# Kernel optimization log

Measured on AMD Instinct MI355X. Metric: run time of the kernel, lower is better.

## Reference

```python
import jax, jax.numpy as jnp
import numpy as np

DIM, E_DIM, HID = 512, 1024, 256
N_EXP, N_MIC, TOP_K, TOP_K_MIC = 8, 325, 2, 8
EPS_LN = 1e-5


def _layernorm(x, g, b):
    mu = x.mean(-1, keepdims=True)
    var = ((x - mu) ** 2).mean(-1, keepdims=True)
    return (x - mu) / jnp.sqrt(var + EPS_LN) * g + b


def setup_inputs() -> dict:
    key = jax.random.key(0)
    ks = jax.random.split(key, 20)
    s = 0.02
    return {
        "x": jax.random.normal(ks[0], (2, 512, DIM), jnp.float32),
        "router_w": jax.random.normal(ks[1], (N_EXP, DIM), jnp.float32) * s,
        "router_b": jnp.zeros((N_EXP,), jnp.float32),
        "exp_w1": jax.random.normal(ks[2], (N_EXP, E_DIM, DIM), jnp.float32) * s,
        "exp_b1": jnp.zeros((N_EXP, E_DIM), jnp.float32),
        "exp_w2": jax.random.normal(ks[3], (N_EXP, DIM, E_DIM), jnp.float32) * s,
        "exp_b2": jnp.zeros((N_EXP, DIM), jnp.float32),
        "mrouter_w": jax.random.normal(ks[4], (N_MIC, DIM), jnp.float32) * s,
        "mrouter_b": jnp.zeros((N_MIC,), jnp.float32),
        "mic_w1": jax.random.normal(ks[5], (N_MIC, HID, DIM), jnp.float32) * s,
        "mic_b1": jnp.zeros((N_MIC, HID), jnp.float32),
        "mic_w2": jax.random.normal(ks[6], (N_MIC, DIM, HID), jnp.float32) * s,
        "mic_b2": jnp.zeros((N_MIC, DIM), jnp.float32),
        "mic_g": jnp.ones((N_MIC, DIM), jnp.float32),
        "mic_beta": jnp.zeros((N_MIC, DIM), jnp.float32),
        "norm_g": jnp.ones((DIM,), jnp.float32),
        "norm_b": jnp.zeros((DIM,), jnp.float32),
    }


def _forward(x, router_w, router_b, exp_w1, exp_b1, exp_w2, exp_b2,
             mrouter_w, mrouter_b, mic_w1, mic_b1, mic_w2, mic_b2,
             mic_g, mic_beta, norm_g, norm_b):
    B, S, D = x.shape
    xf = x.reshape(-1, D)  # [T, D]

    # ---- expert routing (top-2 of 8) ----
    probs = jax.nn.softmax(xf @ router_w.T + router_b, axis=-1)
    topp, topi = jax.lax.top_k(probs, TOP_K)
    topp = topp / (topp.sum(-1, keepdims=True) + 1e-8)

    # dense compute over 8 experts, combine with top-k weights
    h = jax.nn.gelu(jnp.einsum('td,ehd->teh', xf, exp_w1) + exp_b1, approximate=False)
    ye = jnp.einsum('teh,edh->ted', h, exp_w2) + exp_b2  # [T, E, D]
    comb_w = (jax.nn.one_hot(topi, N_EXP, dtype=xf.dtype) * topp[..., None]).sum(1)  # [T, E]
    eo = jnp.einsum('te,ted->td', comb_w, ye)

    # ---- micro routing (top-8 of 325) ----
    mprobs = jax.nn.softmax(eo @ mrouter_w.T + mrouter_b, axis=-1)
    mtopp, mtopi = jax.lax.top_k(mprobs, TOP_K_MIC)
    mtopp = mtopp / (mtopp.sum(-1, keepdims=True) + 1e-8)

    def micro_slot(eo, p, idx):
        # gather per-token micro params, batched GEMV dispatch
        hm = jax.nn.gelu(jnp.einsum('td,thd->th', eo, mic_w1[idx]) + mic_b1[idx],
                         approximate=False)
        ym = jnp.einsum('th,tdh->td', hm, mic_w2[idx]) + mic_b2[idx]
        n = _layernorm(eo + ym, mic_g[idx], mic_beta[idx])
        return p[:, None] * n

    micro_slot = jax.checkpoint(micro_slot, static_argnums=())
    mo = jnp.zeros_like(eo)
    for k in range(TOP_K_MIC):  # small fixed loop over slots
        mo = mo + micro_slot(eo, mtopp[:, k], mtopi[:, k])

    combined = (eo + 0.1 * mo).reshape(B, S, D)
    return _layernorm(combined, norm_g, norm_b)


def reference(x, router_w, router_b, exp_w1, exp_b1, exp_w2, exp_b2,
              mrouter_w, mrouter_b, mic_w1, mic_b1, mic_w2, mic_b2,
              mic_g, mic_beta, norm_g, norm_b):
    return _forward(x, router_w, router_b, exp_w1, exp_b1, exp_w2, exp_b2,
                    mrouter_w, mrouter_b, mic_w1, mic_b1, mic_w2, mic_b2,
                    mic_g, mic_beta, norm_g, norm_b)
```

## Files before the change

kernel.cpp:

```cpp
#include <hip/hip_runtime.h>
#include <hip/hip_bf16.h>
#include <math.h>

#define T_TOK 1024
#define DIMM  512
#define EDIM  1024
#define HIDD  256
#define NEXP  8
#define NMIC  325
#define E8TILES 264
#define MTILES  840

typedef __attribute__((ext_vector_type(8))) short bf16x8;
typedef __attribute__((ext_vector_type(4))) float f32x4;

__device__ __forceinline__ float dot4(float4 a, float4 b) {
    return a.x*b.x + a.y*b.y + a.z*b.z + a.w*b.w;
}
__device__ __forceinline__ float gelu_exact(float x) {
    return 0.5f * x * (1.0f + erff(x * 0.70710678118654752f));
}
__device__ __forceinline__ float wave_sum(float v) {
    #pragma unroll
    for (int o = 32; o; o >>= 1) v += __shfl_xor(v, o);
    return v;
}
__device__ __forceinline__ short f2bf(float f) {
    union { __hip_bfloat16 h; short s; } u;
    u.h = __float2bfloat16(f);
    return u.s;
}
__device__ __forceinline__ bf16x8 cvt8(float4 a, float4 b) {
    bf16x8 r;
    r[0]=f2bf(a.x); r[1]=f2bf(a.y); r[2]=f2bf(a.z); r[3]=f2bf(a.w);
    r[4]=f2bf(b.x); r[5]=f2bf(b.y); r[6]=f2bf(b.z); r[7]=f2bf(b.w);
    return r;
}

__global__ void k_router(const float* __restrict__ x, const float* __restrict__ rw,
                         const float* __restrict__ rb, int* __restrict__ eidx,
                         float* __restrict__ ew, int* __restrict__ ecnt) {
    int wave = threadIdx.x >> 6, lane = threadIdx.x & 63;
    int t = blockIdx.x * 4 + wave;
    if (t >= T_TOK) return;
    const float* xr = x + (size_t)t * DIMM;
    float xv[8];
    #pragma unroll
    for (int j = 0; j < 8; ++j) xv[j] = xr[lane + 64*j];
    float p[NEXP];
    #pragma unroll
    for (int e = 0; e < NEXP; ++e) {
        const float* wr = rw + (size_t)e * DIMM;
        float a = 0.f;
        #pragma unroll
        for (int j = 0; j < 8; ++j) a += xv[j] * wr[lane + 64*j];
        p[e] = wave_sum(a) + rb[e];
    }
    float m = p[0];
    #pragma unroll
    for (int e = 1; e < NEXP; ++e) m = fmaxf(m, p[e]);
    float Z = 0.f;
    #pragma unroll
    for (int e = 0; e < NEXP; ++e) { p[e] = expf(p[e] - m); Z += p[e]; }
    #pragma unroll
    for (int e = 0; e < NEXP; ++e) p[e] /= Z;
    int i1 = 0; float v1 = p[0];
    #pragma unroll
    for (int e = 1; e < NEXP; ++e) if (p[e] > v1) { v1 = p[e]; i1 = e; }
    int i2 = -1; float v2 = -1.f;
    #pragma unroll
    for (int e = 0; e < NEXP; ++e) if (e != i1 && p[e] > v2) { v2 = p[e]; i2 = e; }
    float s = v1 + v2 + 1e-8f;
    if (lane == 0) {
        eidx[t*2] = i1; eidx[t*2+1] = i2;
        ew[t*2] = v1 / s; ew[t*2+1] = v2 / s;
        atomicAdd(&ecnt[i1], 1); atomicAdd(&ecnt[i2], 1);
    }
}

__global__ void k_scan(const int* __restrict__ cnt, int n, int pm,
                       int* __restrict__ off, int* __restrict__ cur,
                       int2* __restrict__ tiles, int* __restrict__ ntile) {
    __shared__ int s[512], s2[512];
    int tid = threadIdx.x;
    int v  = (tid < n) ? cnt[tid] : 0;
    int tc = (v + pm - 1) / pm;
    s[tid] = v; s2[tid] = tc;
    __syncthreads();
    for (int d = 1; d < 512; d <<= 1) {
        int a = (tid >= d) ? s[tid-d] : 0;
        int b = (tid >= d) ? s2[tid-d] : 0;
        __syncthreads();
        s[tid] += a; s2[tid] += b;
        __syncthreads();
    }
    int myoff = s[tid] - v, tb = s2[tid] - tc;
    if (tid < n) { off[tid] = myoff; cur[tid] = myoff; }
    if (tid == n-1) off[n] = s[tid];
    if (tid == 511) *ntile = s2[511];
    for (int j = 0; j < tc; ++j) tiles[tb + j] = make_int2(tid, myoff + j*pm);
}

__global__ void k_scatter(const int* __restrict__ idx, const float* __restrict__ w,
                          int total, int S, int* __restrict__ cur,
                          int* __restrict__ ptok, float* __restrict__ pw) {
    int g = blockIdx.x * blockDim.x + threadIdx.x;
    if (g >= total) return;
    int t = g / S;
    int e = idx[g];
    int pos = atomicAdd(&cur[e], 1);
    ptok[pos] = t; pw[pos] = w[g];
}

__global__ __launch_bounds__(256) void k_effn1(
    const float* __restrict__ x, const float* __restrict__ w1, const float* __restrict__ b1,
    const int2* __restrict__ tiles, const int* __restrict__ ntile,
    const int* __restrict__ eoff, const int* __restrict__ ep_tok,
    float* __restrict__ hbuf) {
    if ((int)blockIdx.x >= *ntile) return;
    int2 tl = tiles[blockIdx.x];
    int e = tl.x, pbase = tl.y;
    int m = min(8, eoff[e+1] - pbase);
    __shared__ float4 xs[8][128];
    __shared__ int tok_s[8];
    int tid = threadIdx.x;
    if (tid < 8) tok_s[tid] = ep_tok[pbase + ((tid < m) ? tid : 0)];
    __syncthreads();
    const float4* x4 = (const float4*)x;
    for (int q = tid; q < 8*128; q += 256) {
        int i = q >> 7, k = q & 127;
        xs[i][k] = x4[(size_t)tok_s[i] * 128 + k];
    }
    __syncthreads();
    int c = blockIdx.y * 256 + tid;
    const float4* wr = (const float4*)(w1 + ((size_t)e * EDIM + c) * DIMM);
    float acc[8];
    #pragma unroll
    for (int i = 0; i < 8; ++i) acc[i] = 0.f;
    for (int kk = 0; kk < 128; ++kk) {
        float4 wv = wr[kk];
        #pragma unroll
        for (int i = 0; i < 8; ++i) acc[i] += dot4(wv, xs[i][kk]);
    }
    float bb = b1[(size_t)e * EDIM + c];
    for (int i = 0; i < m; ++i)
        hbuf[(size_t)(pbase + i) * EDIM + c] = gelu_exact(acc[i] + bb);
}

__global__ __launch_bounds__(256) void k_effn2(
    const float* __restrict__ hbuf, const float* __restrict__ w2, const float* __restrict__ b2,
    const int2* __restrict__ tiles, const int* __restrict__ ntile,
    const int* __restrict__ eoff, const int* __restrict__ ep_tok, const float* __restrict__ ep_w,
    float* __restrict__ eo) {
    if ((int)blockIdx.x >= *ntile) return;
    int2 tl = tiles[blockIdx.x];
    int e = tl.x, pbase = tl.y;
    int m = min(8, eoff[e+1] - pbase);
    int kc = blockIdx.z;
    __shared__ float4 hs[8][128];
    __shared__ int tok_s[8];
    __shared__ float pw_s[8];
    int tid = threadIdx.x;
    if (tid < 8) {
        int ok = tid < m;
        tok_s[tid] = ok ? ep_tok[pbase + tid] : 0;
        pw_s[tid]  = ok ? ep_w[pbase + tid] : 0.f;
    }
    __syncthreads();
    const float4* h4 = (const float4*)hbuf;
    for (int q = tid; q < 8*128; q += 256) {
        int i = q >> 7, k = q & 127;
        hs[i][k] = h4[(size_t)(pbase + ((i < m) ? i : 0)) * 256 + kc * 128 + k];
    }
    __syncthreads();
    int c = blockIdx.y * 256 + tid;
    const float4* wr = (const float4*)(w2 + ((size_t)e * DIMM + c) * EDIM + (size_t)kc * 512);
    float acc[8];
    #pragma unroll
    for (int i = 0; i < 8; ++i) acc[i] = 0.f;
    for (int kk = 0; kk < 128; ++kk) {
        float4 wv = wr[kk];
        #pragma unroll
        for (int i = 0; i < 8; ++i) acc[i] += dot4(wv, hs[i][kk]);
    }
    float bb = (kc == 0) ? b2[(size_t)e * DIMM + c] : 0.f;
    for (int i = 0; i < m; ++i) {
        float val = (acc[i] + bb) * pw_s[i];
        atomicAdd(&eo[(size_t)tok_s[i] * DIMM + c], val);
    }
}

__global__ __launch_bounds__(384) void k_mlog(
    const float* __restrict__ eo, const float* __restrict__ mw, const float* __restrict__ mb,
    float* __restrict__ mlog) {
    int t0 = blockIdx.x * 4;
    __shared__ float4 es[4][128];
    int tid = threadIdx.x;
    const float4* eo4 = (const float4*)eo;
    for (int q = tid; q < 4*128; q += 384) {
        int i = q >> 7, k = q & 127;
        es[i][k] = eo4[(size_t)(t0 + i) * 128 + k];
    }
    __syncthreads();
    if (tid < NMIC) {
        const float4* wr = (const float4*)(mw + (size_t)tid * DIMM);
        float acc[4] = {0.f, 0.f, 0.f, 0.f};
        for (int kk = 0; kk < 128; ++kk) {
            float4 wv = wr[kk];
            #pragma unroll
            for (int i = 0; i < 4; ++i) acc[i] += dot4(wv, es[i][kk]);
        }
        float bb = mb[tid];
        #pragma unroll
        for (int i = 0; i < 4; ++i) mlog[(size_t)(t0 + i) * NMIC + tid] = acc[i] + bb;
    }
}

__global__ void k_mtop(const float* __restrict__ mlog, int* __restrict__ mtopi,
                       float* __restrict__ mtopp, int* __restrict__ mcnt) {
    int wave = threadIdx.x >> 6, lane = threadIdx.x & 63;
    int t = blockIdx.x * 4 + wave;
    if (t >= T_TOK) return;
    float v[6]; int vi[6];
    #pragma unroll
    for (int j = 0; j < 6; ++j) {
        int n = lane + 64*j;
        vi[j] = n;
        v[j] = (n < NMIC) ? mlog[(size_t)t * NMIC + n] : -1e30f;
    }
    float M = v[0];
    #pragma unroll
    for (int j = 1; j < 6; ++j) M = fmaxf(M, v[j]);
    #pragma unroll
    for (int o = 32; o; o >>= 1) M = fmaxf(M, __shfl_xor(M, o));
    float Z = 0.f;
    #pragma unroll
    for (int j = 0; j < 6; ++j) Z += expf(v[j] - M);
    Z = wave_sum(Z);
    float bk[8]; int bi[8];
    for (int k = 0; k < 8; ++k) {
        float lv = v[0]; int li = vi[0];
        #pragma unroll
        for (int j = 1; j < 6; ++j)
            if (v[j] > lv) { lv = v[j]; li = vi[j]; }
        #pragma unroll
        for (int o = 32; o; o >>= 1) {
            float ov = __shfl_xor(lv, o); int oi = __shfl_xor(li, o);
            if (ov > lv || (ov == lv && oi < li)) { lv = ov; li = oi; }
        }
        bk[k] = expf(lv - M) / Z; bi[k] = li;
        #pragma unroll
        for (int j = 0; j < 6; ++j) if (vi[j] == li) v[j] = -1e30f;
    }
    float s = 0.f;
    #pragma unroll
    for (int k = 0; k < 8; ++k) s += bk[k];
    s += 1e-8f;
    if (lane == 0) {
        for (int k = 0; k < 8; ++k) {
            mtopi[t*8 + k] = bi[k];
            mtopp[t*8 + k] = bk[k] / s;
            atomicAdd(&mcnt[bi[k]], 1);
        }
    }
}

__global__ __launch_bounds__(256, 4) void k_micro(
    const float* __restrict__ eo, const float* __restrict__ w1, const float* __restrict__ b1,
    const float* __restrict__ w2, const float* __restrict__ b2,
    const float* __restrict__ g, const float* __restrict__ beta,
    const int2* __restrict__ tiles, const int* __restrict__ ntile,
    const int* __restrict__ moff, const int* __restrict__ mp_tok, const float* __restrict__ mp_w,
    float* __restrict__ mo) {
    if ((int)blockIdx.x >= *ntile) return;
    int2 tl = tiles[blockIdx.x];
    int mi = tl.x, pbase = tl.y;
    int pm = min(16, moff[mi+1] - pbase);
    __shared__ __align__(16) char smem[34816];
    short* hf  = (short*)smem;
    short* eof = (short*)(smem + 8192);
    float* R   = (float*)smem;
    __shared__ int tok_s[16];
    __shared__ float pw_s[16];
    int tid = threadIdx.x;
    if (tid < 16) {
        int ok = tid < pm;
        tok_s[tid] = mp_tok[pbase + (ok ? tid : 0)];
        pw_s[tid]  = ok ? mp_w[pbase + tid] : 0.f;
    }
    __syncthreads();
    int m0 = tid & 15;
    const float4* eorow = (const float4*)(eo + (size_t)tok_s[m0] * DIMM);
    for (int kk = tid >> 4; kk < 128; kk += 16) {
        float4 v = eorow[kk];
        int off = ((kk >> 3) * 512) + ((((kk >> 1) & 3) * 16 + m0) * 8) + ((kk & 1) * 4);
        short4 s4; s4.x = f2bf(v.x); s4.y = f2bf(v.y); s4.z = f2bf(v.z); s4.w = f2bf(v.w);
        *(short4*)(eof + off) = s4;
    }
    __syncthreads();
    int wave = tid >> 6, lane = tid & 63;
    int quad = lane >> 4, lcol = lane & 15;
    f32x4 zero = {0.f, 0.f, 0.f, 0.f};
    f32x4 accA[4];
    #pragma unroll
    for (int q = 0; q < 4; ++q) accA[q] = zero;
    const float* w1base = w1 + (size_t)mi * HIDD * DIMM;
    for (int ks = 0; ks < 16; ++ks) {
        bf16x8 a = *(bf16x8*)(eof + ks*512 + lane*8);
        int kb = ks*32 + quad*8;
        #pragma unroll
        for (int q = 0; q < 4; ++q) {
            int n = wave*64 + q*16 + lcol;
            const float* wp = w1base + (size_t)n * DIMM + kb;
            float4 wa = *(const float4*)wp;
            float4 wb = *(const float4*)(wp + 4);
            accA[q] = __builtin_amdgcn_mfma_f32_16x16x32_bf16(a, cvt8(wa, wb), accA[q], 0, 0, 0);
        }
    }
    #pragma unroll
    for (int q = 0; q < 4; ++q) {
        int h = wave*64 + q*16 + lcol;
        float bb = b1[(size_t)mi * HIDD + h];
        int obase = ((h >> 5) * 512) + (((h >> 3) & 3) * 16) * 8 + (h & 7);
        #pragma unroll
        for (int r = 0; r < 4; ++r) {
            int mm = quad*4 + r;
            hf[obase + mm*8] = f2bf(gelu_exact(accA[q][r] + bb));
        }
    }
    __syncthreads();
    f32x4 accB[8];
    #pragma unroll
    for (int q = 0; q < 8; ++q) accB[q] = zero;
    const float* w2base = w2 + (size_t)mi * DIMM * HIDD;
    for (int ks = 0; ks < 8; ++ks) {
        bf16x8 a = *(bf16x8*)(hf + ks*512 + lane*8);
        int kb = ks*32 + quad*8;
        #pragma unroll
        for (int q = 0; q < 8; ++q) {
            int d = wave*128 + q*16 + lcol;
            const float* wp = w2base + (size_t)d * HIDD + kb;
            float4 wa = *(const float4*)wp;
            float4 wb = *(const float4*)(wp + 4);
            accB[q] = __builtin_amdgcn_mfma_f32_16x16x32_bf16(a, cvt8(wa, wb), accB[q], 0, 0, 0);
        }
    }
    __syncthreads();
    #pragma unroll
    for (int q = 0; q < 8; ++q) {
        int d = wave*128 + q*16 + lcol;
        float bb = b2[(size_t)mi * DIMM + d];
        #pragma unroll
        for (int r = 0; r < 4; ++r) {
            int mm = quad*4 + r;
            R[mm*520 + d] = accB[q][r] + bb;
        }
    }
    __syncthreads();
    for (int i = wave; i < pm; i += 4) {
        int t = tok_s[i];
        const float* eort = eo + (size_t)t * DIMM;
        float vv[8];
        float sum = 0.f;
        #pragma unroll
        for (int j = 0; j < 8; ++j) {
            int d = lane + 64*j;
            vv[j] = R[i*520 + d] + eort[d];
            sum += vv[j];
        }
        sum = wave_sum(sum);
        float mu = sum * (1.f/512.f);
        float var = 0.f;
        #pragma unroll
        for (int j = 0; j < 8; ++j) { float d0 = vv[j] - mu; var += d0*d0; }
        var = wave_sum(var) * (1.f/512.f);
        float rstd = rsqrtf(var + 1e-5f);
        float p = pw_s[i];
        #pragma unroll
        for (int j = 0; j < 8; ++j) {
            int d = lane + 64*j;
            float nj = (vv[j] - mu) * rstd * g[(size_t)mi * DIMM + d] + beta[(size_t)mi * DIMM + d];
            atomicAdd(&mo[(size_t)t * DIMM + d], p * nj);
        }
    }
}

__global__ void k_final(const float* __restrict__ eo, const float* __restrict__ mo,
                        const float* __restrict__ g, const float* __restrict__ b,
                        float* __restrict__ out) {
    int wave = threadIdx.x >> 6, lane = threadIdx.x & 63;
    int t = blockIdx.x * 4 + wave;
    if (t >= T_TOK) return;
    float vv[8];
    float sum = 0.f;
    #pragma unroll
    for (int j = 0; j < 8; ++j) {
        int d = lane + 64*j;
        vv[j] = eo[(size_t)t * DIMM + d] + 0.1f * mo[(size_t)t * DIMM + d];
        sum += vv[j];
    }
    sum = wave_sum(sum);
    float mu = sum * (1.f/512.f);
    float var = 0.f;
    #pragma unroll
    for (int j = 0; j < 8; ++j) { float d0 = vv[j] - mu; var += d0*d0; }
    var = wave_sum(var) * (1.f/512.f);
    float rstd = rsqrtf(var + 1e-5f);
    #pragma unroll
    for (int j = 0; j < 8; ++j) {
        int d = lane + 64*j;
        out[(size_t)t * DIMM + d] = (vv[j] - mu) * rstd * g[d] + b[d];
    }
}

extern "C" void kernel_launch(void* const* d_in, const int* in_sizes, int n_in,
                              void* d_out, int out_size, void* d_ws, size_t ws_size,
                              hipStream_t stream) {
    const float* x    = (const float*)d_in[0];
    const float* rw   = (const float*)d_in[1];
    const float* rb   = (const float*)d_in[2];
    const float* ew1  = (const float*)d_in[3];
    const float* eb1  = (const float*)d_in[4];
    const float* ew2  = (const float*)d_in[5];
    const float* eb2  = (const float*)d_in[6];
    const float* mrw  = (const float*)d_in[7];
    const float* mrb  = (const float*)d_in[8];
    const float* mw1  = (const float*)d_in[9];
    const float* mb1  = (const float*)d_in[10];
    const float* mw2  = (const float*)d_in[11];
    const float* mb2  = (const float*)d_in[12];
    const float* mg   = (const float*)d_in[13];
    const float* mbeta= (const float*)d_in[14];
    const float* ng   = (const float*)d_in[15];
    const float* nb   = (const float*)d_in[16];
    float* out = (float*)d_out;

    char* w = (char*)d_ws;
    auto alloc = [&](size_t bytes) -> char* {
        char* p = w;
        w += (bytes + 255) & ~(size_t)255;
        return p;
    };
    float* eo    = (float*)alloc((size_t)T_TOK * DIMM * 4);
    float* mo    = (float*)alloc((size_t)T_TOK * DIMM * 4);
    float* hbuf  = (float*)alloc((size_t)2048 * EDIM * 4);
    float* mlog  = (float*)alloc((size_t)T_TOK * NMIC * 4);
    float* ewts  = (float*)alloc(2048 * 4);
    float* mtopp = (float*)alloc(8192 * 4);
    float* ep_w  = (float*)alloc(2048 * 4);
    float* mp_w  = (float*)alloc(8192 * 4);
    int*   eidx  = (int*)alloc(2048 * 4);
    int*   mtopi = (int*)alloc(8192 * 4);
    int*   cnts  = (int*)alloc((NEXP + NMIC) * 4);
    int*   ecnt  = cnts;
    int*   mcnt  = cnts + NEXP;
    int*   eoff  = (int*)alloc((NEXP + 1) * 4);
    int*   ecur  = (int*)alloc(NEXP * 4);
    int*   moff  = (int*)alloc((NMIC + 1) * 4);
    int*   mcur  = (int*)alloc(NMIC * 4);
    int2*  etile = (int2*)alloc(E8TILES * 8);
    int2*  mtile = (int2*)alloc(MTILES * 8);
    int*   entile= (int*)alloc(4);
    int*   mntile= (int*)alloc(4);
    int*   ep_tok= (int*)alloc(2048 * 4);
    int*   mp_tok= (int*)alloc(8192 * 4);

    hipMemsetAsync(eo, 0, (size_t)2 * T_TOK * DIMM * 4, stream);
    hipMemsetAsync(cnts, 0, (NEXP + NMIC) * 4, stream);

    k_router <<<T_TOK/4, 256, 0, stream>>>(x, rw, rb, eidx, ewts, ecnt);
    k_scan   <<<1, 512, 0, stream>>>(ecnt, NEXP, 8, eoff, ecur, etile, entile);
    k_scatter<<<(T_TOK*2 + 255)/256, 256, 0, stream>>>(eidx, ewts, T_TOK*2, 2, ecur, ep_tok, ep_w);
    k_effn1  <<<dim3(E8TILES, 4, 1), 256, 0, stream>>>(x, ew1, eb1, etile, entile, eoff, ep_tok, hbuf);
    k_effn2  <<<dim3(E8TILES, 2, 2), 256, 0, stream>>>(hbuf, ew2, eb2, etile, entile, eoff, ep_tok, ep_w, eo);
    k_mlog   <<<T_TOK/4, 384, 0, stream>>>(eo, mrw, mrb, mlog);
    k_mtop   <<<T_TOK/4, 256, 0, stream>>>(mlog, mtopi, mtopp, mcnt);
    k_scan   <<<1, 512, 0, stream>>>(mcnt, NMIC, 16, moff, mcur, mtile, mntile);
    k_scatter<<<(T_TOK*8 + 255)/256, 256, 0, stream>>>(mtopi, mtopp, T_TOK*8, 8, mcur, mp_tok, mp_w);
    k_micro  <<<MTILES, 256, 0, stream>>>(eo, mw1, mb1, mw2, mb2, mg, mbeta,
                                          mtile, mntile, moff, mp_tok, mp_w, mo);
    k_final  <<<T_TOK/4, 256, 0, stream>>>(eo, mo, ng, nb, out);
}
```

Measured before the change: 718.4 us.

## Split micro-expert kernel into three stages and widen expert token tiles

The fused micro-expert kernel is split into three stages, each launched on a 2x wider grid. The first computes half of the hidden units per block and stores them as bf16 in a global buffer that reuses hbuf. The second computes half of the output columns into a per-pair y buffer, and a separate per-pair LayerNorm kernel does the residual add, normalisation and atomic accumulation. The aim is more parallel blocks and less register and LDS pressure per block. In exchange it adds global round trips for the intermediates and, for the dense experts, tiles grow from 8 to 16 tokens so weight rows are reused across more tokens, at higher register use.

```diff
diff --git a/kernel.cpp b/kernel.cpp
--- a/kernel.cpp
+++ b/kernel.cpp
@@ -8,8 +8,9 @@
 #define HIDD  256
 #define NEXP  8
 #define NMIC  325
-#define E8TILES 264
+#define E16TILES 136
 #define MTILES  840
+#define NPAIR_M 8192
 
 typedef __attribute__((ext_vector_type(8))) short bf16x8;
 typedef __attribute__((ext_vector_type(4))) float f32x4;
@@ -103,13 +104,14 @@
 
 __global__ void k_scatter(const int* __restrict__ idx, const float* __restrict__ w,
                           int total, int S, int* __restrict__ cur,
-                          int* __restrict__ ptok, float* __restrict__ pw) {
+                          int* __restrict__ ptok, float* __restrict__ pw,
+                          int* __restrict__ pmi) {
     int g = blockIdx.x * blockDim.x + threadIdx.x;
     if (g >= total) return;
     int t = g / S;
     int e = idx[g];
     int pos = atomicAdd(&cur[e], 1);
-    ptok[pos] = t; pw[pos] = w[g];
+    ptok[pos] = t; pw[pos] = w[g]; pmi[pos] = e;
 }
 
 __global__ __launch_bounds__(256) void k_effn1(
@@ -120,27 +122,27 @@
     if ((int)blockIdx.x >= *ntile) return;
     int2 tl = tiles[blockIdx.x];
     int e = tl.x, pbase = tl.y;
-    int m = min(8, eoff[e+1] - pbase);
-    __shared__ float4 xs[8][128];
-    __shared__ int tok_s[8];
+    int m = min(16, eoff[e+1] - pbase);
+    __shared__ float4 xs[16][128];
+    __shared__ int tok_s[16];
     int tid = threadIdx.x;
-    if (tid < 8) tok_s[tid] = ep_tok[pbase + ((tid < m) ? tid : 0)];
+    if (tid < 16) tok_s[tid] = ep_tok[pbase + ((tid < m) ? tid : 0)];
     __syncthreads();
     const float4* x4 = (const float4*)x;
-    for (int q = tid; q < 8*128; q += 256) {
+    for (int q = tid; q < 16*128; q += 256) {
         int i = q >> 7, k = q & 127;
         xs[i][k] = x4[(size_t)tok_s[i] * 128 + k];
     }
     __syncthreads();
     int c = blockIdx.y * 256 + tid;
     const float4* wr = (const float4*)(w1 + ((size_t)e * EDIM + c) * DIMM);
-    float acc[8];
-    #pragma unroll
-    for (int i = 0; i < 8; ++i) acc[i] = 0.f;
+    float acc[16];
+    #pragma unroll
+    for (int i = 0; i < 16; ++i) acc[i] = 0.f;
     for (int kk = 0; kk < 128; ++kk) {
         float4 wv = wr[kk];
         #pragma unroll
-        for (int i = 0; i < 8; ++i) acc[i] += dot4(wv, xs[i][kk]);
+        for (int i = 0; i < 16; ++i) acc[i] += dot4(wv, xs[i][kk]);
     }
     float bb = b1[(size_t)e * EDIM + c];
     for (int i = 0; i < m; ++i)
@@ -155,33 +157,33 @@
     if ((int)blockIdx.x >= *ntile) return;
     int2 tl = tiles[blockIdx.x];
     int e = tl.x, pbase = tl.y;
-    int m = min(8, eoff[e+1] - pbase);
+    int m = min(16, eoff[e+1] - pbase);
     int kc = blockIdx.z;
-    __shared__ float4 hs[8][128];
-    __shared__ int tok_s[8];
-    __shared__ float pw_s[8];
+    __shared__ float4 hs[16][128];
+    __shared__ int tok_s[16];
+    __shared__ float pw_s[16];
     int tid = threadIdx.x;
-    if (tid < 8) {
+    if (tid < 16) {
         int ok = tid < m;
         tok_s[tid] = ok ? ep_tok[pbase + tid] : 0;
         pw_s[tid]  = ok ? ep_w[pbase + tid] : 0.f;
     }
     __syncthreads();
     const float4* h4 = (const float4*)hbuf;
-    for (int q = tid; q < 8*128; q += 256) {
+    for (int q = tid; q < 16*128; q += 256) {
         int i = q >> 7, k = q & 127;
         hs[i][k] = h4[(size_t)(pbase + ((i < m) ? i : 0)) * 256 + kc * 128 + k];
     }
     __syncthreads();
     int c = blockIdx.y * 256 + tid;
     const float4* wr = (const float4*)(w2 + ((size_t)e * DIMM + c) * EDIM + (size_t)kc * 512);
-    float acc[8];
-    #pragma unroll
-    for (int i = 0; i < 8; ++i) acc[i] = 0.f;
+    float acc[16];
+    #pragma unroll
+    for (int i = 0; i < 16; ++i) acc[i] = 0.f;
     for (int kk = 0; kk < 128; ++kk) {
         float4 wv = wr[kk];
         #pragma unroll
-        for (int i = 0; i < 8; ++i) acc[i] += dot4(wv, hs[i][kk]);
+        for (int i = 0; i < 16; ++i) acc[i] += dot4(wv, hs[i][kk]);
     }
     float bb = (kc == 0) ? b2[(size_t)e * DIMM + c] : 0.f;
     for (int i = 0; i < m; ++i) {
@@ -265,29 +267,21 @@
     }
 }
 
-__global__ __launch_bounds__(256, 4) void k_micro(
+__global__ __launch_bounds__(256) void k_mffn1(
     const float* __restrict__ eo, const float* __restrict__ w1, const float* __restrict__ b1,
-    const float* __restrict__ w2, const float* __restrict__ b2,
-    const float* __restrict__ g, const float* __restrict__ beta,
     const int2* __restrict__ tiles, const int* __restrict__ ntile,
-    const int* __restrict__ moff, const int* __restrict__ mp_tok, const float* __restrict__ mp_w,
-    float* __restrict__ mo) {
+    const int* __restrict__ moff, const int* __restrict__ mp_tok,
+    short* __restrict__ ghbuf) {
     if ((int)blockIdx.x >= *ntile) return;
     int2 tl = tiles[blockIdx.x];
     int mi = tl.x, pbase = tl.y;
     int pm = min(16, moff[mi+1] - pbase);
-    __shared__ __align__(16) char smem[34816];
-    short* hf  = (short*)smem;
-    short* eof = (short*)(smem + 8192);
-    float* R   = (float*)smem;
+    int by = blockIdx.y;
+    __shared__ __align__(16) short eof[8192];
+    __shared__ __align__(16) short hf[2048];
     __shared__ int tok_s[16];
-    __shared__ float pw_s[16];
     int tid = threadIdx.x;
-    if (tid < 16) {
-        int ok = tid < pm;
-        tok_s[tid] = mp_tok[pbase + (ok ? tid : 0)];
-        pw_s[tid]  = ok ? mp_w[pbase + tid] : 0.f;
-    }
+    if (tid < 16) tok_s[tid] = mp_tok[pbase + ((tid < pm) ? tid : 0)];
     __syncthreads();
     int m0 = tid & 15;
     const float4* eorow = (const float4*)(eo + (size_t)tok_s[m0] * DIMM);
@@ -301,16 +295,15 @@
     int wave = tid >> 6, lane = tid & 63;
     int quad = lane >> 4, lcol = lane & 15;
     f32x4 zero = {0.f, 0.f, 0.f, 0.f};
-    f32x4 accA[4];
-    #pragma unroll
-    for (int q = 0; q < 4; ++q) accA[q] = zero;
+    f32x4 accA[2];
+    accA[0] = zero; accA[1] = zero;
     const float* w1base = w1 + (size_t)mi * HIDD * DIMM;
     for (int ks = 0; ks < 16; ++ks) {
         bf16x8 a = *(bf16x8*)(eof + ks*512 + lane*8);
         int kb = ks*32 + quad*8;
         #pragma unroll
-        for (int q = 0; q < 4; ++q) {
-            int n = wave*64 + q*16 + lcol;
+        for (int q = 0; q < 2; ++q) {
+            int n = by*128 + wave*32 + q*16 + lcol;
             const float* wp = w1base + (size_t)n * DIMM + kb;
             float4 wa = *(const float4*)wp;
             float4 wb = *(const float4*)(wp + 4);
@@ -318,10 +311,10 @@
         }
     }
     #pragma unroll
-    for (int q = 0; q < 4; ++q) {
-        int h = wave*64 + q*16 + lcol;
-        float bb = b1[(size_t)mi * HIDD + h];
-        int obase = ((h >> 5) * 512) + (((h >> 3) & 3) * 16) * 8 + (h & 7);
+    for (int q = 0; q < 2; ++q) {
+        int hp = wave*32 + q*16 + lcol;
+        float bb = b1[(size_t)mi * HIDD + by*128 + hp];
+        int obase = ((hp >> 5) * 512) + (((hp >> 3) & 3) * 16) * 8 + (hp & 7);
         #pragma unroll
         for (int r = 0; r < 4; ++r) {
             int mm = quad*4 + r;
@@ -329,59 +322,83 @@
         }
     }
     __syncthreads();
-    f32x4 accB[8];
-    #pragma unroll
-    for (int q = 0; q < 8; ++q) accB[q] = zero;
+    short* gh = ghbuf + (size_t)blockIdx.x * 4096 + (size_t)by * 2048;
+    ((int4*)gh)[tid] = ((const int4*)hf)[tid];
+}
+
+__global__ __launch_bounds__(256) void k_mffn2(
+    const short* __restrict__ ghbuf, const float* __restrict__ w2, const float* __restrict__ b2,
+    const int2* __restrict__ tiles, const int* __restrict__ ntile, const int* __restrict__ moff,
+    float* __restrict__ ybuf) {
+    if ((int)blockIdx.x >= *ntile) return;
+    int2 tl = tiles[blockIdx.x];
+    int mi = tl.x, pbase = tl.y;
+    int pm = min(16, moff[mi+1] - pbase);
+    int by = blockIdx.y;
+    int tid = threadIdx.x, wave = tid >> 6, lane = tid & 63;
+    int quad = lane >> 4, lcol = lane & 15;
+    const short* gh = ghbuf + (size_t)blockIdx.x * 4096;
+    f32x4 zero = {0.f, 0.f, 0.f, 0.f};
+    f32x4 accB[4];
+    #pragma unroll
+    for (int q = 0; q < 4; ++q) accB[q] = zero;
     const float* w2base = w2 + (size_t)mi * DIMM * HIDD;
     for (int ks = 0; ks < 8; ++ks) {
-        bf16x8 a = *(bf16x8*)(hf + ks*512 + lane*8);
+        bf16x8 a = *(const bf16x8*)(gh + ks*512 + lane*8);
         int kb = ks*32 + quad*8;
         #pragma unroll
-        for (int q = 0; q < 8; ++q) {
-            int d = wave*128 + q*16 + lcol;
+        for (int q = 0; q < 4; ++q) {
+            int d = by*256 + wave*64 + q*16 + lcol;
             const float* wp = w2base + (size_t)d * HIDD + kb;
             float4 wa = *(const float4*)wp;
             float4 wb = *(const float4*)(wp + 4);
             accB[q] = __builtin_amdgcn_mfma_f32_16x16x32_bf16(a, cvt8(wa, wb), accB[q], 0, 0, 0);
         }
     }
-    __syncthreads();
-    #pragma unroll
-    for (int q = 0; q < 8; ++q) {
-        int d = wave*128 + q*16 + lcol;
+    #pragma unroll
+    for (int q = 0; q < 4; ++q) {
+        int d = by*256 + wave*64 + q*16 + lcol;
         float bb = b2[(size_t)mi * DIMM + d];
         #pragma unroll
         for (int r = 0; r < 4; ++r) {
             int mm = quad*4 + r;
-            R[mm*520 + d] = accB[q][r] + bb;
-        }
-    }
-    __syncthreads();
-    for (int i = wave; i < pm; i += 4) {
-        int t = tok_s[i];
-        const float* eort = eo + (size_t)t * DIMM;
-        float vv[8];
-        float sum = 0.f;
-        #pragma unroll
-        for (int j = 0; j < 8; ++j) {
-            int d = lane + 64*j;
-            vv[j] = R[i*520 + d] + eort[d];
-            sum += vv[j];
-        }
-        sum = wave_sum(sum);
-        float mu = sum * (1.f/512.f);
-        float var = 0.f;
-        #pragma unroll
-        for (int j = 0; j < 8; ++j) { float d0 = vv[j] - mu; var += d0*d0; }
-        var = wave_sum(var) * (1.f/512.f);
-        float rstd = rsqrtf(var + 1e-5f);
-        float p = pw_s[i];
-        #pragma unroll
-        for (int j = 0; j < 8; ++j) {
-            int d = lane + 64*j;
-            float nj = (vv[j] - mu) * rstd * g[(size_t)mi * DIMM + d] + beta[(size_t)mi * DIMM + d];
-            atomicAdd(&mo[(size_t)t * DIMM + d], p * nj);
-        }
+            if (mm < pm) ybuf[(size_t)(pbase + mm) * DIMM + d] = accB[q][r] + bb;
+        }
+    }
+}
+
+__global__ __launch_bounds__(256) void k_mln(
+    const float* __restrict__ ybuf, const float* __restrict__ eo,
+    const float* __restrict__ g, const float* __restrict__ beta,
+    const int* __restrict__ mp_tok, const float* __restrict__ mp_w,
+    const int* __restrict__ mp_mi, float* __restrict__ mo) {
+    int wave = threadIdx.x >> 6, lane = threadIdx.x & 63;
+    int p = blockIdx.x * 4 + wave;
+    int t = mp_tok[p];
+    int mi = mp_mi[p];
+    float pw = mp_w[p];
+    const float* yr = ybuf + (size_t)p * DIMM;
+    const float* er = eo + (size_t)t * DIMM;
+    float vv[8];
+    float sum = 0.f;
+    #pragma unroll
+    for (int j = 0; j < 8; ++j) {
+        int d = lane + 64*j;
+        vv[j] = yr[d] + er[d];
+        sum += vv[j];
+    }
+    sum = wave_sum(sum);
+    float mu = sum * (1.f/512.f);
+    float var = 0.f;
+    #pragma unroll
+    for (int j = 0; j < 8; ++j) { float d0 = vv[j] - mu; var += d0*d0; }
+    var = wave_sum(var) * (1.f/512.f);
+    float rstd = rsqrtf(var + 1e-5f);
+    #pragma unroll
+    for (int j = 0; j < 8; ++j) {
+        int d = lane + 64*j;
+        float nj = (vv[j] - mu) * rstd * g[(size_t)mi * DIMM + d] + beta[(size_t)mi * DIMM + d];
+        atomicAdd(&mo[(size_t)t * DIMM + d], pw * nj);
     }
 }
 
@@ -444,6 +461,7 @@
     float* eo    = (float*)alloc((size_t)T_TOK * DIMM * 4);
     float* mo    = (float*)alloc((size_t)T_TOK * DIMM * 4);
     float* hbuf  = (float*)alloc((size_t)2048 * EDIM * 4);
+    float* ybuf  = (float*)alloc((size_t)NPAIR_M * DIMM * 4);
     float* mlog  = (float*)alloc((size_t)T_TOK * NMIC * 4);
     float* ewts  = (float*)alloc(2048 * 4);
     float* mtopp = (float*)alloc(8192 * 4);
@@ -458,26 +476,30 @@
     int*   ecur  = (int*)alloc(NEXP * 4);
     int*   moff  = (int*)alloc((NMIC + 1) * 4);
     int*   mcur  = (int*)alloc(NMIC * 4);
-    int2*  etile = (int2*)alloc(E8TILES * 8);
+    int2*  etile = (int2*)alloc(E16TILES * 8);
     int2*  mtile = (int2*)alloc(MTILES * 8);
     int*   entile= (int*)alloc(4);
     int*   mntile= (int*)alloc(4);
     int*   ep_tok= (int*)alloc(2048 * 4);
     int*   mp_tok= (int*)alloc(8192 * 4);
+    int*   ep_mi = (int*)alloc(2048 * 4);
+    int*   mp_mi = (int*)alloc(8192 * 4);
+    short* ghbuf = (short*)hbuf;
 
     hipMemsetAsync(eo, 0, (size_t)2 * T_TOK * DIMM * 4, stream);
     hipMemsetAsync(cnts, 0, (NEXP + NMIC) * 4, stream);
 
     k_router <<<T_TOK/4, 256, 0, stream>>>(x, rw, rb, eidx, ewts, ecnt);
-    k_scan   <<<1, 512, 0, stream>>>(ecnt, NEXP, 8, eoff, ecur, etile, entile);
-    k_scatter<<<(T_TOK*2 + 255)/256, 256, 0, stream>>>(eidx, ewts, T_TOK*2, 2, ecur, ep_tok, ep_w);
-    k_effn1  <<<dim3(E8TILES, 4, 1), 256, 0, stream>>>(x, ew1, eb1, etile, entile, eoff, ep_tok, hbuf);
-    k_effn2  <<<dim3(E8TILES, 2, 2), 256, 0, stream>>>(hbuf, ew2, eb2, etile, entile, eoff, ep_tok, ep_w, eo);
+    k_scan   <<<1, 512, 0, stream>>>(ecnt, NEXP, 16, eoff, ecur, etile, entile);
+    k_scatter<<<(T_TOK*2 + 255)/256, 256, 0, stream>>>(eidx, ewts, T_TOK*2, 2, ecur, ep_tok, ep_w, ep_mi);
+    k_effn1  <<<dim3(E16TILES, 4, 1), 256, 0, stream>>>(x, ew1, eb1, etile, entile, eoff, ep_tok, hbuf);
+    k_effn2  <<<dim3(E16TILES, 2, 2), 256, 0, stream>>>(hbuf, ew2, eb2, etile, entile, eoff, ep_tok, ep_w, eo);
     k_mlog   <<<T_TOK/4, 384, 0, stream>>>(eo, mrw, mrb, mlog);
     k_mtop   <<<T_TOK/4, 256, 0, stream>>>(mlog, mtopi, mtopp, mcnt);
     k_scan   <<<1, 512, 0, stream>>>(mcnt, NMIC, 16, moff, mcur, mtile, mntile);
-    k_scatter<<<(T_TOK*8 + 255)/256, 256, 0, stream>>>(mtopi, mtopp, T_TOK*8, 8, mcur, mp_tok, mp_w);
-    k_micro  <<<MTILES, 256, 0, stream>>>(eo, mw1, mb1, mw2, mb2, mg, mbeta,
-                                          mtile, mntile, moff, mp_tok, mp_w, mo);
+    k_scatter<<<(T_TOK*8 + 255)/256, 256, 0, stream>>>(mtopi, mtopp, T_TOK*8, 8, mcur, mp_tok, mp_w, mp_mi);
+    k_mffn1  <<<dim3(MTILES, 2, 1), 256, 0, stream>>>(eo, mw1, mb1, mtile, mntile, moff, mp_tok, ghbuf);
+    k_mffn2  <<<dim3(MTILES, 2, 1), 256, 0, stream>>>(ghbuf, mw2, mb2, mtile, mntile, moff, ybuf);
+    k_mln    <<<NPAIR_M/4, 256, 0, stream>>>(ybuf, eo, mg, mbeta, mp_tok, mp_w, mp_mi, mo);
     k_final  <<<T_TOK/4, 256, 0, stream>>>(eo, mo, ng, nb, out);
 }
```

Result: no change. 724.0 us (+0.8%).
